# Optimization experiments

Hardware: AMD Instinct MI355X
Metric: run time of the kernel (lower is better)

## Reference

```python
import jax, jax.numpy as jnp
import numpy as np

B, T, H = 2048, 784, 64
STATE_DIM = 1
IN_DIM = 1 + STATE_DIM  # concat([t, y])
INNER_LR = 0.01
NUM_GRAD_STEPS = 4


def _unif(k, shape, fan_in):
    lim = 1.0 / np.sqrt(fan_in)
    return jax.random.uniform(k, shape, jnp.float32, -lim, lim)


def setup_inputs() -> dict:
    key = jax.random.key(0)
    ks = jax.random.split(key, 8)
    ts = (jnp.arange(T, dtype=jnp.float32) / T)
    xs = jax.random.normal(ks[0], (B, T), jnp.float32)
    mask = jax.random.bernoulli(ks[1], 0.5, (B, T - 1))  # teacher-forcing draws
    # equinox Linear default init: U(-1/sqrt(fan_in), 1/sqrt(fan_in)) for W and b
    W1 = _unif(ks[2], (H, IN_DIM), IN_DIM)
    b1 = _unif(ks[3], (H,), IN_DIM)
    W2 = _unif(ks[4], (H, H), H)
    b2 = _unif(ks[5], (H,), H)
    W3 = _unif(ks[6], (STATE_DIM, H), H)
    b3 = _unif(ks[7], (STATE_DIM,), H)
    return {"ts": ts, "xs": xs, "mask": mask,
            "W1": W1, "b1": b1, "W2": W2, "b2": b2, "W3": W3, "b3": b3}


def _mlp(theta, t, y):
    # theta: tuple of (W1,b1,W2,b2,W3,b3); t, y scalars -> output (state_dim,)
    W1, b1, W2, b2, W3, b3 = theta
    h = jnp.stack([t, y])                # (2,)
    h = jnp.tanh(W1 @ h + b1)            # (H,)
    h = jnp.tanh(W2 @ h + b2)            # (H,)
    return W3 @ h + b3                   # (state_dim,)


def reference(ts, xs, mask, W1, b1, W2, b2, W3, b3):
    theta0 = (W1, b1, W2, b2, W3, b3)

    def forward(xs_row, mask_row):
        def step(carry, inp):
            theta, t_prev, x_hat, x_prev = carry
            x_true, t_curr, m = inp
            x_t = jnp.where(m, x_true, x_hat)  # bernoulli(0.5) teacher forcing

            def inner_loss(th):
                pred = _mlp(th, t_curr, x_prev)
                return jnp.mean((pred - x_t) ** 2)

            for _ in range(NUM_GRAD_STEPS):
                g = jax.grad(inner_loss)(theta)
                theta = jax.tree_util.tree_map(
                    lambda p, gr: p - INNER_LR * gr, theta, g)

            deltat = t_curr - t_prev
            x_hat_new = _mlp(theta, t_curr + deltat, x_true).squeeze()
            return (theta, t_curr, x_hat_new, x_true), x_hat_new

        init = (theta0, ts[0], xs_row[0], xs_row[0])
        _, x_hats = jax.lax.scan(step, init, (xs_row[1:], ts[1:], mask_row))
        return jnp.concatenate([xs_row[:1], x_hats], axis=0)  # (T,)

    return jax.vmap(forward)(xs, mask)  # (B, T)
```

## Files before the change

kernel.cpp:

```cpp
#include <hip/hip_runtime.h>
#include <math.h>


#define TT  784
#define HH  64
#define LR  0.01f

typedef _Float16 h2v __attribute__((ext_vector_type(2)));
#define FDOT2(a, b, c) __builtin_amdgcn_fdot2((a), (b), (c), false)
#define BC(f) __builtin_bit_cast(h2v, (f))

__device__ __forceinline__ float fast_tanh(float x) {
    float e = __builtin_amdgcn_exp2f(x * 2.885390081777926814f);
    float r = __builtin_amdgcn_rcpf(e + 1.0f);
    return fmaf(-2.0f, r, 1.0f);
}

template <int CTRL, int RMASK, bool BC_>
__device__ __forceinline__ float dpp_add(float x) {
    int t = __builtin_amdgcn_update_dpp(0, __builtin_bit_cast(int, x),
                                        CTRL, RMASK, 0xf, BC_);
    return x + __builtin_bit_cast(float, t);
}

__device__ __forceinline__ float wave_sum(float x) {
    x = dpp_add<0x111, 0xf, true>(x);
    x = dpp_add<0x112, 0xf, true>(x);
    x = dpp_add<0x114, 0xf, true>(x);
    x = dpp_add<0x118, 0xf, true>(x);
    x = dpp_add<0x142, 0xa, false>(x);
    x = dpp_add<0x143, 0xc, false>(x);
    return __builtin_bit_cast(float,
        __builtin_amdgcn_readlane(__builtin_bit_cast(int, x), 63));
}

__global__ __launch_bounds__(64, 2)
void ttt_kernel(const float* __restrict__ ts,
                const float* __restrict__ xs,
                const int*   __restrict__ mask,
                const float* __restrict__ W1,
                const float* __restrict__ b1,
                const float* __restrict__ W2,
                const float* __restrict__ b2,
                const float* __restrict__ W3,
                const float* __restrict__ b3,
                float* __restrict__ out)
{
    __shared__ __align__(16) _Float16 s_h1h[HH];
    __shared__ __align__(16) _Float16 s_dzh[HH];
    __shared__ float s_ts[TT];
    __shared__ float s_xs[TT];
    __shared__ int   s_mask[TT - 1];

    const int row  = blockIdx.x;
    const int lane = threadIdx.x;

    for (int i = lane; i < TT; i += HH) {
        s_ts[i] = ts[i];
        s_xs[i] = xs[row * TT + i];
    }
    for (int i = lane; i < TT - 1; i += HH) s_mask[i] = mask[row * (TT - 1) + i];

    float w1a = W1[2 * lane + 0];
    float w1b = W1[2 * lane + 1];
    float b1v = b1[lane];
    float b2v = b2[lane];
    float w3v = W3[lane];
    float b3v = b3[0];

    h2v w2r[HH / 2];
    h2v w2c[HH / 2];
#pragma unroll
    for (int k = 0; k < HH / 2; ++k) {
        w2r[k] = h2v{(_Float16)W2[lane * HH + 2 * k], (_Float16)W2[lane * HH + 2 * k + 1]};
        w2c[k] = h2v{(_Float16)W2[(2 * k) * HH + lane], (_Float16)W2[(2 * k + 1) * HH + lane]};
    }
    __syncthreads();

    const float4* h1v4 = (const float4*)s_h1h;
    const float4* dzv4 = (const float4*)s_dzh;

    float t_prev = s_ts[0];
    const float x0 = s_xs[0];
    float x_hat  = x0;
    float x_prev = x0;
    if (lane == 0) out[row * TT] = x0;

    float4 hr[8];
    float  h1f, h2f, predf;
    h2v    sdv_p = h2v{(_Float16)0.f, (_Float16)0.f};

    auto FWD = [&](float tin, float xin, bool apply) {
        float z1 = fmaf(w1a, tin, fmaf(w1b, xin, b1v));
        h1f = fast_tanh(z1);
        s_h1h[lane] = (_Float16)h1f;
        if (apply) {
#pragma unroll
            for (int k = 0; k < 8; ++k) {
                float4 q = hr[k];
                w2r[4 * k + 0] += sdv_p * BC(q.x);
                w2r[4 * k + 1] += sdv_p * BC(q.y);
                w2r[4 * k + 2] += sdv_p * BC(q.z);
                w2r[4 * k + 3] += sdv_p * BC(q.w);
            }
        }
        float a0 = 0.f, a1 = 0.f, a2 = 0.f, a3 = 0.f;
#pragma unroll
        for (int k = 0; k < 8; ++k) {
            float4 q = h1v4[k];
            hr[k] = q;
            a0 = FDOT2(w2r[4 * k + 0], BC(q.x), a0);
            a1 = FDOT2(w2r[4 * k + 1], BC(q.y), a1);
            a2 = FDOT2(w2r[4 * k + 2], BC(q.z), a2);
            a3 = FDOT2(w2r[4 * k + 3], BC(q.w), a3);
        }
        float z2 = ((a0 + a1) + (a2 + a3)) + b2v;
        h2f = fast_tanh(z2);
        predf = wave_sum(w3v * h2f) + b3v;
    };

    auto BWD = [&](float tin, float xin, float xt) {
        const float dl   = 2.0f * (predf - xt);
        const float dz2s = dl * w3v * (1.0f - h2f * h2f);
        s_dzh[lane] = (_Float16)dz2s;
        w3v = fmaf(-LR * dl, h2f, w3v);
        b3v -= LR * dl;
        b2v -= LR * dz2s;
        const _Float16 sh = (_Float16)(-LR * h1f);
        const h2v shv = h2v{sh, sh};
        float d0 = 0.f, d1 = 0.f, d2 = 0.f, d3 = 0.f;
#pragma unroll
        for (int k = 0; k < 8; ++k) {
            float4 q = dzv4[k];
            h2v q0 = BC(q.x), q1 = BC(q.y), q2 = BC(q.z), q3 = BC(q.w);
            d0 = FDOT2(w2c[4 * k + 0], q0, d0);
            d1 = FDOT2(w2c[4 * k + 1], q1, d1);
            d2 = FDOT2(w2c[4 * k + 2], q2, d2);
            d3 = FDOT2(w2c[4 * k + 3], q3, d3);
            w2c[4 * k + 0] += shv * q0;
            w2c[4 * k + 1] += shv * q1;
            w2c[4 * k + 2] += shv * q2;
            w2c[4 * k + 3] += shv * q3;
        }
        const float dh1 = (d0 + d1) + (d2 + d3);
        const float dz1 = dh1 * (1.0f - h1f * h1f);
        w1a = fmaf(-LR * dz1, tin, w1a);
        w1b = fmaf(-LR * dz1, xin, w1b);
        b1v -= LR * dz1;
        const _Float16 sd = (_Float16)(-LR * dz2s);
        sdv_p = h2v{sd, sd};
    };

    FWD(s_ts[1], x0, false);

    for (int t = 1; t < TT; ++t) {
        const float tc     = s_ts[t];
        const float x_true = s_xs[t];
        const int   m      = s_mask[t - 1];
        const float x_t    = m ? x_true : x_hat;

        BWD(tc, x_prev, x_t);
        for (int gs = 1; gs < 4; ++gs) {
            FWD(tc, x_prev, true);
            BWD(tc, x_prev, x_t);
        }

        const float tin = tc + (tc - t_prev);
        FWD(tin, x_true, true);
        x_hat = predf;

        if (lane == 0) out[row * TT + t] = x_hat;
        t_prev = tc;
        x_prev = x_true;
    }
}

extern "C" void kernel_launch(void* const* d_in, const int* in_sizes, int n_in,
                              void* d_out, int out_size, void* d_ws, size_t ws_size,
                              hipStream_t stream) {
    const float* ts   = (const float*)d_in[0];
    const float* xs   = (const float*)d_in[1];
    const int*   mask = (const int*)d_in[2];
    const float* W1   = (const float*)d_in[3];
    const float* b1   = (const float*)d_in[4];
    const float* W2   = (const float*)d_in[5];
    const float* b2   = (const float*)d_in[6];
    const float* W3   = (const float*)d_in[7];
    const float* b3   = (const float*)d_in[8];
    float* out = (float*)d_out;

    const int B = in_sizes[1] / TT;
    dim3 grid(B), block(HH);
    hipLaunchKernelGGL(ttt_kernel, grid, block, 0, stream,
                       ts, xs, mask, W1, b1, W2, b2, W3, b3, out);
}
```

Before: 2.553 ms.

## Process two independent batch rows per wavefront to interleave dependency chains

Each 64-lane block now handles two batch rows, with separate per-row weight copies kept in registers and their forward/backward steps interleaved. The goal is instruction-level parallelism: the serial latency of LDS round-trips, DPP reductions and tanh chains in one row can overlap with work from the other. The cost is roughly double the VGPR footprint (two fp16 copies of W2 rows and columns), with launch bounds relaxed to one block per unit. The grid is halved, and the code assumes an even B.

```diff
diff --git a/kernel.cpp b/kernel.cpp
--- a/kernel.cpp
+++ b/kernel.cpp
@@ -5,6 +5,7 @@
 #define TT  784
 #define HH  64
 #define LR  0.01f
+#define NR  2
 
 typedef _Float16 h2v __attribute__((ext_vector_type(2)));
 #define FDOT2(a, b, c) __builtin_amdgcn_fdot2((a), (b), (c), false)
@@ -34,7 +35,7 @@
         __builtin_amdgcn_readlane(__builtin_bit_cast(int, x), 63));
 }
 
-__global__ __launch_bounds__(64, 2)
+__global__ __launch_bounds__(64, 1)
 void ttt_kernel(const float* __restrict__ ts,
                 const float* __restrict__ xs,
                 const int*   __restrict__ mask,
@@ -46,132 +47,164 @@
                 const float* __restrict__ b3,
                 float* __restrict__ out)
 {
-    __shared__ __align__(16) _Float16 s_h1h[HH];
-    __shared__ __align__(16) _Float16 s_dzh[HH];
+    __shared__ __align__(16) _Float16 s_h1h[NR][HH];
+    __shared__ __align__(16) _Float16 s_dzh[NR][HH];
     __shared__ float s_ts[TT];
-    __shared__ float s_xs[TT];
-    __shared__ int   s_mask[TT - 1];
-
-    const int row  = blockIdx.x;
+    __shared__ float s_xs[NR][TT];
+    __shared__ int   s_mask[NR][TT - 1];
+
+    const int blk  = blockIdx.x;
     const int lane = threadIdx.x;
+    const int rowA = 2 * blk;
 
     for (int i = lane; i < TT; i += HH) {
         s_ts[i] = ts[i];
-        s_xs[i] = xs[row * TT + i];
-    }
-    for (int i = lane; i < TT - 1; i += HH) s_mask[i] = mask[row * (TT - 1) + i];
-
-    float w1a = W1[2 * lane + 0];
-    float w1b = W1[2 * lane + 1];
-    float b1v = b1[lane];
-    float b2v = b2[lane];
-    float w3v = W3[lane];
-    float b3v = b3[0];
-
-    h2v w2r[HH / 2];
-    h2v w2c[HH / 2];
-#pragma unroll
-    for (int k = 0; k < HH / 2; ++k) {
-        w2r[k] = h2v{(_Float16)W2[lane * HH + 2 * k], (_Float16)W2[lane * HH + 2 * k + 1]};
-        w2c[k] = h2v{(_Float16)W2[(2 * k) * HH + lane], (_Float16)W2[(2 * k + 1) * HH + lane]};
+        s_xs[0][i] = xs[rowA * TT + i];
+        s_xs[1][i] = xs[(rowA + 1) * TT + i];
+    }
+    for (int i = lane; i < TT - 1; i += HH) {
+        s_mask[0][i] = mask[rowA * (TT - 1) + i];
+        s_mask[1][i] = mask[(rowA + 1) * (TT - 1) + i];
+    }
+
+    float w1a[NR], w1b[NR], b1v[NR], b2v[NR], w3v[NR], b3v[NR];
+    h2v   w2r[NR][HH / 2];
+    h2v   w2c[NR][HH / 2];
+    {
+        const float a = W1[2 * lane + 0], b = W1[2 * lane + 1];
+        const float c = b1[lane], d = b2[lane], e = W3[lane], f = b3[0];
+#pragma unroll
+        for (int r = 0; r < NR; ++r) {
+            w1a[r] = a; w1b[r] = b; b1v[r] = c;
+            b2v[r] = d; w3v[r] = e; b3v[r] = f;
+        }
+#pragma unroll
+        for (int k = 0; k < HH / 2; ++k) {
+            h2v vr = h2v{(_Float16)W2[lane * HH + 2 * k],
+                         (_Float16)W2[lane * HH + 2 * k + 1]};
+            h2v vc = h2v{(_Float16)W2[(2 * k) * HH + lane],
+                         (_Float16)W2[(2 * k + 1) * HH + lane]};
+            w2r[0][k] = vr; w2r[1][k] = vr;
+            w2c[0][k] = vc; w2c[1][k] = vc;
+        }
     }
     __syncthreads();
 
-    const float4* h1v4 = (const float4*)s_h1h;
-    const float4* dzv4 = (const float4*)s_dzh;
-
     float t_prev = s_ts[0];
-    const float x0 = s_xs[0];
-    float x_hat  = x0;
-    float x_prev = x0;
-    if (lane == 0) out[row * TT] = x0;
-
-    float4 hr[8];
-    float  h1f, h2f, predf;
-    h2v    sdv_p = h2v{(_Float16)0.f, (_Float16)0.f};
-
-    auto FWD = [&](float tin, float xin, bool apply) {
-        float z1 = fmaf(w1a, tin, fmaf(w1b, xin, b1v));
-        h1f = fast_tanh(z1);
-        s_h1h[lane] = (_Float16)h1f;
+    float x_hat[NR], x_prev[NR];
+#pragma unroll
+    for (int r = 0; r < NR; ++r) {
+        x_hat[r] = s_xs[r][0];
+        x_prev[r] = s_xs[r][0];
+    }
+    if (lane == 0) {
+        out[rowA * TT] = x_hat[0];
+        out[(rowA + 1) * TT] = x_hat[1];
+    }
+
+    float4 hr[NR][8];
+    float  h1f[NR], h2f[NR], predf[NR];
+    h2v    sdv_p[NR];
+#pragma unroll
+    for (int r = 0; r < NR; ++r) sdv_p[r] = h2v{(_Float16)0.f, (_Float16)0.f};
+
+    auto FWD = [&](int r, float tin, float xin, bool apply) {
+        float z1 = fmaf(w1a[r], tin, fmaf(w1b[r], xin, b1v[r]));
+        h1f[r] = fast_tanh(z1);
+        s_h1h[r][lane] = (_Float16)h1f[r];
+        const float4* h1v4 = (const float4*)s_h1h[r];
         if (apply) {
 #pragma unroll
             for (int k = 0; k < 8; ++k) {
-                float4 q = hr[k];
-                w2r[4 * k + 0] += sdv_p * BC(q.x);
-                w2r[4 * k + 1] += sdv_p * BC(q.y);
-                w2r[4 * k + 2] += sdv_p * BC(q.z);
-                w2r[4 * k + 3] += sdv_p * BC(q.w);
+                float4 q = hr[r][k];
+                w2r[r][4 * k + 0] += sdv_p[r] * BC(q.x);
+                w2r[r][4 * k + 1] += sdv_p[r] * BC(q.y);
+                w2r[r][4 * k + 2] += sdv_p[r] * BC(q.z);
+                w2r[r][4 * k + 3] += sdv_p[r] * BC(q.w);
             }
         }
         float a0 = 0.f, a1 = 0.f, a2 = 0.f, a3 = 0.f;
 #pragma unroll
         for (int k = 0; k < 8; ++k) {
             float4 q = h1v4[k];
-            hr[k] = q;
-            a0 = FDOT2(w2r[4 * k + 0], BC(q.x), a0);
-            a1 = FDOT2(w2r[4 * k + 1], BC(q.y), a1);
-            a2 = FDOT2(w2r[4 * k + 2], BC(q.z), a2);
-            a3 = FDOT2(w2r[4 * k + 3], BC(q.w), a3);
-        }
-        float z2 = ((a0 + a1) + (a2 + a3)) + b2v;
-        h2f = fast_tanh(z2);
-        predf = wave_sum(w3v * h2f) + b3v;
+            hr[r][k] = q;
+            a0 = FDOT2(w2r[r][4 * k + 0], BC(q.x), a0);
+            a1 = FDOT2(w2r[r][4 * k + 1], BC(q.y), a1);
+            a2 = FDOT2(w2r[r][4 * k + 2], BC(q.z), a2);
+            a3 = FDOT2(w2r[r][4 * k + 3], BC(q.w), a3);
+        }
+        float z2 = ((a0 + a1) + (a2 + a3)) + b2v[r];
+        h2f[r] = fast_tanh(z2);
+        predf[r] = wave_sum(w3v[r] * h2f[r]) + b3v[r];
     };
 
-    auto BWD = [&](float tin, float xin, float xt) {
-        const float dl   = 2.0f * (predf - xt);
-        const float dz2s = dl * w3v * (1.0f - h2f * h2f);
-        s_dzh[lane] = (_Float16)dz2s;
-        w3v = fmaf(-LR * dl, h2f, w3v);
-        b3v -= LR * dl;
-        b2v -= LR * dz2s;
-        const _Float16 sh = (_Float16)(-LR * h1f);
+    auto BWD = [&](int r, float tin, float xin, float xt) {
+        const float dl   = 2.0f * (predf[r] - xt);
+        const float dz2s = dl * w3v[r] * (1.0f - h2f[r] * h2f[r]);
+        s_dzh[r][lane] = (_Float16)dz2s;
+        const float4* dzv4 = (const float4*)s_dzh[r];
+        w3v[r] = fmaf(-LR * dl, h2f[r], w3v[r]);
+        b3v[r] -= LR * dl;
+        b2v[r] -= LR * dz2s;
+        const _Float16 sh = (_Float16)(-LR * h1f[r]);
         const h2v shv = h2v{sh, sh};
         float d0 = 0.f, d1 = 0.f, d2 = 0.f, d3 = 0.f;
 #pragma unroll
         for (int k = 0; k < 8; ++k) {
             float4 q = dzv4[k];
             h2v q0 = BC(q.x), q1 = BC(q.y), q2 = BC(q.z), q3 = BC(q.w);
-            d0 = FDOT2(w2c[4 * k + 0], q0, d0);
-            d1 = FDOT2(w2c[4 * k + 1], q1, d1);
-            d2 = FDOT2(w2c[4 * k + 2], q2, d2);
-            d3 = FDOT2(w2c[4 * k + 3], q3, d3);
-            w2c[4 * k + 0] += shv * q0;
-            w2c[4 * k + 1] += shv * q1;
-            w2c[4 * k + 2] += shv * q2;
-            w2c[4 * k + 3] += shv * q3;
+            d0 = FDOT2(w2c[r][4 * k + 0], q0, d0);
+            d1 = FDOT2(w2c[r][4 * k + 1], q1, d1);
+            d2 = FDOT2(w2c[r][4 * k + 2], q2, d2);
+            d3 = FDOT2(w2c[r][4 * k + 3], q3, d3);
+            w2c[r][4 * k + 0] += shv * q0;
+            w2c[r][4 * k + 1] += shv * q1;
+            w2c[r][4 * k + 2] += shv * q2;
+            w2c[r][4 * k + 3] += shv * q3;
         }
         const float dh1 = (d0 + d1) + (d2 + d3);
-        const float dz1 = dh1 * (1.0f - h1f * h1f);
-        w1a = fmaf(-LR * dz1, tin, w1a);
-        w1b = fmaf(-LR * dz1, xin, w1b);
-        b1v -= LR * dz1;
+        const float dz1 = dh1 * (1.0f - h1f[r] * h1f[r]);
+        w1a[r] = fmaf(-LR * dz1, tin, w1a[r]);
+        w1b[r] = fmaf(-LR * dz1, xin, w1b[r]);
+        b1v[r] -= LR * dz1;
         const _Float16 sd = (_Float16)(-LR * dz2s);
-        sdv_p = h2v{sd, sd};
+        sdv_p[r] = h2v{sd, sd};
     };
 
-    FWD(s_ts[1], x0, false);
+    FWD(0, s_ts[1], x_prev[0], false);
+    FWD(1, s_ts[1], x_prev[1], false);
 
     for (int t = 1; t < TT; ++t) {
-        const float tc     = s_ts[t];
-        const float x_true = s_xs[t];
-        const int   m      = s_mask[t - 1];
-        const float x_t    = m ? x_true : x_hat;
-
-        BWD(tc, x_prev, x_t);
+        const float tc = s_ts[t];
+        float x_true[NR], x_t[NR];
+#pragma unroll
+        for (int r = 0; r < NR; ++r) {
+            x_true[r] = s_xs[r][t];
+            x_t[r] = s_mask[r][t - 1] ? x_true[r] : x_hat[r];
+        }
+
+        BWD(0, tc, x_prev[0], x_t[0]);
+        BWD(1, tc, x_prev[1], x_t[1]);
         for (int gs = 1; gs < 4; ++gs) {
-            FWD(tc, x_prev, true);
-            BWD(tc, x_prev, x_t);
+            FWD(0, tc, x_prev[0], true);
+            FWD(1, tc, x_prev[1], true);
+            BWD(0, tc, x_prev[0], x_t[0]);
+            BWD(1, tc, x_prev[1], x_t[1]);
         }
 
         const float tin = tc + (tc - t_prev);
-        FWD(tin, x_true, true);
-        x_hat = predf;
-
-        if (lane == 0) out[row * TT + t] = x_hat;
+        FWD(0, tin, x_true[0], true);
+        FWD(1, tin, x_true[1], true);
+        x_hat[0] = predf[0];
+        x_hat[1] = predf[1];
+
+        if (lane == 0) {
+            out[rowA * TT + t] = x_hat[0];
+            out[(rowA + 1) * TT + t] = x_hat[1];
+        }
         t_prev = tc;
-        x_prev = x_true;
+        x_prev[0] = x_true[0];
+        x_prev[1] = x_true[1];
     }
 }
 
@@ -190,7 +223,7 @@
     float* out = (float*)d_out;
 
     const int B = in_sizes[1] / TT;
-    dim3 grid(B), block(HH);
+    dim3 grid(B / NR), block(HH);
     hipLaunchKernelGGL(ttt_kernel, grid, block, 0, stream,
                        ts, xs, mask, W1, b1, W2, b2, W3, b3, out);
 }
```

After: 3.010 ms. +17.9%, slower.
